# Performance work log

Hardware: AMD Instinct MI355X
Metric: run time of the kernel (lower is better)

Reference implementation:

```python
import jax, jax.numpy as jnp
import numpy as np

N_HEAD = 16

def setup_inputs() -> dict:
    key = jax.random.key(0)
    ks = jax.random.split(key, 9)
    B, T, C = 4, 2048, 1024
    s = 1.0 / np.sqrt(C)
    return {
        "x":  jax.random.normal(ks[0], (B, T, C), jnp.float32),
        "Wq": jax.random.normal(ks[1], (C, C), jnp.float32) * s,
        "bq": jax.random.normal(ks[2], (C,), jnp.float32) * 0.02,
        "Wk": jax.random.normal(ks[3], (C, C), jnp.float32) * s,
        "bk": jax.random.normal(ks[4], (C,), jnp.float32) * 0.02,
        "Wv": jax.random.normal(ks[5], (C, C), jnp.float32) * s,
        "bv": jax.random.normal(ks[6], (C,), jnp.float32) * 0.02,
        "Wp": jax.random.normal(ks[7], (C, C), jnp.float32) * s,
        "bp": jax.random.normal(ks[8], (C,), jnp.float32) * 0.02,
    }

def reference(x, Wq, bq, Wk, bk, Wv, bv, Wp, bp):
    B, T, C = x.shape
    H, D = N_HEAD, C // N_HEAD
    # torch nn.Linear: y = x @ W^T + b
    q = (x @ Wq.T + bq).reshape(B, T, H, D).transpose(0, 2, 1, 3)  # [B,H,T,D]
    k = (x @ Wk.T + bk).reshape(B, T, H, D).transpose(0, 2, 1, 3)
    v = (x @ Wv.T + bv).reshape(B, T, H, D).transpose(0, 2, 1, 3)
    # full TxT causal attention (non-flash path)
    att = jnp.einsum('bhtd,bhsd->bhts', q, k) * (1.0 / np.sqrt(D))  # [B,H,T,T]
    causal = jnp.tril(jnp.ones((T, T), dtype=bool))
    att = jnp.where(causal[None, None], att, -jnp.inf)
    att = jax.nn.softmax(att, axis=-1)
    y = jnp.einsum('bhts,bhsd->bhtd', att, v)  # [B,H,T,D]
    y = y.transpose(0, 2, 1, 3).reshape(B, T, C)
    return y @ Wp.T + bp
```

## Files before the change

kernel.cpp:

```cpp
#include <hip/hip_runtime.h>

typedef __bf16 bf16_t;
typedef __bf16 bf16x8 __attribute__((ext_vector_type(8)));
typedef __bf16 bf16x4 __attribute__((ext_vector_type(4)));
typedef float f32x4 __attribute__((ext_vector_type(4)));
typedef unsigned short ushort_t;

#define T_SEQ 2048
#define C_DIM 1024
#define NH    16
#define HD    64

__device__ __forceinline__ ushort_t f2bf(float f) {
    unsigned u = __builtin_bit_cast(unsigned, f);
    u += 0x7FFFu + ((u >> 16) & 1u);
    return (ushort_t)(u >> 16);
}

__device__ __forceinline__ void async_cp16(const void* g, void* l) {
    __builtin_amdgcn_global_load_lds(
        (const __attribute__((address_space(1))) void*)g,
        (__attribute__((address_space(3))) void*)l, 16, 0, 0);
}

#define X4  2097152
#define W4  262144
__global__ __launch_bounds__(256)
void cvt_all_kernel(const float* __restrict__ x,  const float* __restrict__ Wq,
                    const float* __restrict__ Wk, const float* __restrict__ Wv,
                    ushort_t* __restrict__ xb,  ushort_t* __restrict__ Wqb,
                    ushort_t* __restrict__ Wkb, ushort_t* __restrict__ Wvb) {
    int i = blockIdx.x * 256 + threadIdx.x;
    const float* src; ushort_t* dst; int off;
    if (i < X4)                { src = x;  dst = xb;  off = i; }
    else if (i < X4 + W4)      { src = Wq; dst = Wqb; off = i - X4; }
    else if (i < X4 + 2 * W4)  { src = Wk; dst = Wkb; off = i - X4 - W4; }
    else                       { src = Wv; dst = Wvb; off = i - X4 - 2 * W4; }
    float4 f = ((const float4*)src)[off];
    ushort4 u;
    u.x = f2bf(f.x); u.y = f2bf(f.y); u.z = f2bf(f.z); u.w = f2bf(f.w);
    ((ushort4*)dst)[off] = u;
}

__global__ __launch_bounds__(256)
void cvt_wp_kernel(const float* __restrict__ Wp, ushort_t* __restrict__ Wpb) {
    int i = blockIdx.x * 256 + threadIdx.x;
    float4 f = ((const float4*)Wp)[i];
    ushort4 u;
    u.x = f2bf(f.x); u.y = f2bf(f.y); u.z = f2bf(f.z); u.w = f2bf(f.w);
    ((ushort4*)Wpb)[i] = u;
}

__device__ __forceinline__ void gemm_core_128(const bf16_t* __restrict__ A,
                                              const bf16_t* __restrict__ B,
                                              f32x4 (&acc)[4][4]) {
    __shared__ alignas(16) ushort_t As[128 * 64];
    __shared__ alignas(16) ushort_t Ws[128 * 64];
    const int tid  = threadIdx.x;
    const int lane = tid & 63;
    const int wv   = tid >> 6;
    const int wm   = wv >> 1, wn = wv & 1;
    const int quad = lane >> 4, ln = lane & 15;
    const int m0 = blockIdx.x * 128, n0 = blockIdx.y * 128;

    f32x4 z4 = {0.f, 0.f, 0.f, 0.f};
#pragma unroll
    for (int i = 0; i < 4; i++)
#pragma unroll
        for (int j = 0; j < 4; j++) acc[i][j] = z4;

    const int lr = lane >> 3;
    const int lc = (lane & 7) ^ lr;
    const bf16_t* Ab = A + (size_t)(m0 + wv * 32 + lr) * 1024 + lc * 8;
    const bf16_t* Bb = B + (size_t)(n0 + wv * 32 + lr) * 1024 + lc * 8;

    for (int kt = 0; kt < 1024; kt += 64) {
#pragma unroll
        for (int p = 0; p < 4; ++p) {
            async_cp16(Ab + (size_t)p * 8192 + kt, &As[(wv * 4 + p) * 512]);
            async_cp16(Bb + (size_t)p * 8192 + kt, &Ws[(wv * 4 + p) * 512]);
        }
        __syncthreads();
#pragma unroll
        for (int ks = 0; ks < 2; ++ks) {
            bf16x8 af[4], bfr[4];
#pragma unroll
            for (int i = 0; i < 4; i++)
                af[i] = *(const bf16x8*)&As[(wm * 64 + i * 16 + ln) * 64 +
                                            (((ks * 4 + quad) ^ (ln & 7)) * 8)];
#pragma unroll
            for (int j = 0; j < 4; j++)
                bfr[j] = *(const bf16x8*)&Ws[(wn * 64 + j * 16 + ln) * 64 +
                                             (((ks * 4 + quad) ^ (ln & 7)) * 8)];
#pragma unroll
            for (int i = 0; i < 4; i++)
#pragma unroll
                for (int j = 0; j < 4; j++)
                    acc[i][j] = __builtin_amdgcn_mfma_f32_16x16x32_bf16(af[i], bfr[j],
                                                                        acc[i][j], 0, 0, 0);
        }
        __syncthreads();
    }
}

__global__ __launch_bounds__(256, 3)
void qkv_gemm_kernel(const bf16_t* __restrict__ xb,
                     const bf16_t* __restrict__ Wqb, const float* __restrict__ bq,
                     const bf16_t* __restrict__ Wkb, const float* __restrict__ bk,
                     const bf16_t* __restrict__ Wvb, const float* __restrict__ bv,
                     ushort_t* __restrict__ Qo, ushort_t* __restrict__ Ko,
                     ushort_t* __restrict__ Vo) {
    const int z = blockIdx.z;
    const bf16_t* W   = (z == 0) ? Wqb : (z == 1) ? Wkb : Wvb;
    const float* bias = (z == 0) ? bq : (z == 1) ? bk : bv;
    ushort_t* outp    = (z == 0) ? Qo : (z == 1) ? Ko : Vo;
    const float fs    = (z == 0) ? 0.18033688011112042f : 1.0f;

    f32x4 acc[4][4];
    gemm_core_128(xb, W, acc);

    const int tid  = threadIdx.x;
    const int lane = tid & 63;
    const int wv2  = tid >> 6;
    const int wm   = wv2 >> 1, wn = wv2 & 1;
    const int quad = lane >> 4, ln = lane & 15;
    const int mbase = blockIdx.x * 128 + wm * 64;
    const int nbase = blockIdx.y * 128 + wn * 64;

#pragma unroll
    for (int j = 0; j < 4; j++) {
        int n = nbase + j * 16 + ln;
        float bj = bias[n];
        int h = n >> 6, d = n & 63;
#pragma unroll
        for (int i = 0; i < 4; i++) {
            int mr = mbase + i * 16 + quad * 4;
            int b = mr >> 11;
            int t = mr & 2047;
            if (z < 2) {
                ushort_t* op = outp + ((size_t)(b * NH + h) * T_SEQ + t) * HD + d;
#pragma unroll
                for (int r = 0; r < 4; r++)
                    op[(size_t)r * HD] = f2bf((acc[i][j][r] + bj) * fs);
            } else {
                ushort4 us;
                us.x = f2bf(acc[i][j][0] + bj);
                us.y = f2bf(acc[i][j][1] + bj);
                us.z = f2bf(acc[i][j][2] + bj);
                us.w = f2bf(acc[i][j][3] + bj);
                *(ushort4*)(outp + ((size_t)(b * NH + h) * HD + d) * T_SEQ + t) = us;
            }
        }
    }
}

__device__ __forceinline__ int vkpos(int s) {
    return 32 * (s >> 5) + 8 * ((s >> 2) & 3) + 4 * ((s >> 4) & 1) + (s & 3);
}

__global__ __launch_bounds__(256, 4)
void flash_kernel(const ushort_t* __restrict__ Qw, const ushort_t* __restrict__ Kw,
                  const ushort_t* __restrict__ Vt, ushort_t* __restrict__ Y) {
    __shared__ alignas(16) ushort_t Ks[64 * 72];
    __shared__ alignas(16) ushort_t Vts[64 * 72];

    const int tid  = threadIdx.x;
    const int lane = tid & 63;
    const int wv   = tid >> 6;
    const int quad = lane >> 4, ln = lane & 15;
    const int L  = blockIdx.y * 16 + blockIdx.x;
    const int m  = L >> 3;
    const int bh = ((m >> 4) << 3) | (L & 7);
    const int p  = m & 15;
    const int qa = p, qb = 31 - p;
    const int b = bh >> 4, h = bh & 15;

    bf16x8 ones;
#pragma unroll
    for (int i = 0; i < 8; i++) ones[i] = (bf16_t)1.0f;

    const ushort_t* qpa = Qw + ((size_t)bh * T_SEQ + qa * 64 + wv * 16 + ln) * HD;
    const ushort_t* qpb = Qw + ((size_t)bh * T_SEQ + qb * 64 + wv * 16 + ln) * HD;
    bf16x8 aqA0 = *(const bf16x8*)(qpa + quad * 8);
    bf16x8 aqA1 = *(const bf16x8*)(qpa + 32 + quad * 8);
    bf16x8 aqB0 = *(const bf16x8*)(qpb + quad * 8);
    bf16x8 aqB1 = *(const bf16x8*)(qpb + 32 + quad * 8);

    f32x4 oA[4], oB[4];
    f32x4 z4 = {0.f, 0.f, 0.f, 0.f};
#pragma unroll
    for (int i = 0; i < 4; i++) { oA[i] = z4; oB[i] = z4; }
    f32x4 lA4 = z4, lB4 = z4;

    const int row0 = tid >> 3, c80 = (tid & 7) * 8;
    const int row1 = (256 + tid) >> 3;
    const int kp0 = vkpos(c80);
    const int kp1 = vkpos(c80 + 4);

    uint4 pk0, pk1, pv0, pv1;
    pk0 = *(const uint4*)(Kw + ((size_t)bh * T_SEQ + row0) * HD + c80);
    pv0 = *(const uint4*)(Vt + ((size_t)bh * HD + row0) * T_SEQ + c80);
    pk1 = *(const uint4*)(Kw + ((size_t)bh * T_SEQ + row1) * HD + c80);
    pv1 = *(const uint4*)(Vt + ((size_t)bh * HD + row1) * T_SEQ + c80);

    const int qrow = wv * 16 + ln;

    for (int st = 0; st <= qb; ++st) {
        __syncthreads();
        *(uint4*)&Ks[row0 * 72 + c80] = pk0;
        *(uint4*)&Ks[row1 * 72 + c80] = pk1;
        {
            uint2 a0 = {pv0.x, pv0.y}, a1 = {pv0.z, pv0.w};
            uint2 b0 = {pv1.x, pv1.y}, b1 = {pv1.z, pv1.w};
            *(uint2*)&Vts[row0 * 72 + kp0] = a0;
            *(uint2*)&Vts[row0 * 72 + kp1] = a1;
            *(uint2*)&Vts[row1 * 72 + kp0] = b0;
            *(uint2*)&Vts[row1 * 72 + kp1] = b1;
        }
        if (st < qb) {
            int s1 = (st + 1) * 64;
            pk0 = *(const uint4*)(Kw + ((size_t)bh * T_SEQ + s1 + row0) * HD + c80);
            pv0 = *(const uint4*)(Vt + ((size_t)bh * HD + row0) * T_SEQ + s1 + c80);
            pk1 = *(const uint4*)(Kw + ((size_t)bh * T_SEQ + s1 + row1) * HD + c80);
            pv1 = *(const uint4*)(Vt + ((size_t)bh * HD + row1) * T_SEQ + s1 + c80);
        }
        __syncthreads();

        const bool doA = (st <= qa);
        const bool dgA = (st == qa), dgB = (st == qb);

        bf16x8 apA[2], apB[2];
#pragma unroll
        for (int n16 = 0; n16 < 4; n16++) {
            bf16x8 bk0 = *(const bf16x8*)&Ks[(n16 * 16 + ln) * 72 + quad * 8];
            bf16x8 bk1 = *(const bf16x8*)&Ks[(n16 * 16 + ln) * 72 + 32 + quad * 8];
            const int ks = n16 >> 1, hf = (n16 & 1) * 4;
            f32x4 zB = {0.f, 0.f, 0.f, 0.f};
            zB = __builtin_amdgcn_mfma_f32_16x16x32_bf16(bk0, aqB0, zB, 0, 0, 0);
            zB = __builtin_amdgcn_mfma_f32_16x16x32_bf16(bk1, aqB1, zB, 0, 0, 0);
            if (doA) {
                f32x4 zA = {0.f, 0.f, 0.f, 0.f};
                zA = __builtin_amdgcn_mfma_f32_16x16x32_bf16(bk0, aqA0, zA, 0, 0, 0);
                zA = __builtin_amdgcn_mfma_f32_16x16x32_bf16(bk1, aqA1, zA, 0, 0, 0);
#pragma unroll
                for (int r = 0; r < 4; r++) {
                    float v = zA[r];
                    v = (dgA && (n16 * 16 + quad * 4 + r > qrow)) ? -1e30f : v;
                    apA[ks][hf + r] = (bf16_t)__builtin_amdgcn_exp2f(v);
                }
            }
#pragma unroll
            for (int r = 0; r < 4; r++) {
                float v = zB[r];
                v = (dgB && (n16 * 16 + quad * 4 + r > qrow)) ? -1e30f : v;
                apB[ks][hf + r] = (bf16_t)__builtin_amdgcn_exp2f(v);
            }
        }

#pragma unroll
        for (int ks = 0; ks < 2; ks++) {
            if (doA)
                lA4 = __builtin_amdgcn_mfma_f32_16x16x32_bf16(apA[ks], ones, lA4, 0, 0, 0);
            lB4 = __builtin_amdgcn_mfma_f32_16x16x32_bf16(apB[ks], ones, lB4, 0, 0, 0);
#pragma unroll
            for (int d16 = 0; d16 < 4; d16++) {
                bf16x8 bv = *(const bf16x8*)&Vts[(d16 * 16 + ln) * 72 + ks * 32 + quad * 8];
                if (doA)
                    oA[d16] = __builtin_amdgcn_mfma_f32_16x16x32_bf16(apA[ks], bv, oA[d16], 0, 0, 0);
                oB[d16] = __builtin_amdgcn_mfma_f32_16x16x32_bf16(apB[ks], bv, oB[d16], 0, 0, 0);
            }
        }
    }

#pragma unroll
    for (int ph = 0; ph < 2; ph++) {
        f32x4* o = ph ? oB : oA;
        f32x4 l4 = ph ? lB4 : lA4;
        int qt = ph ? qb : qa;
        f32x4 inv = {1.f / l4[0], 1.f / l4[1], 1.f / l4[2], 1.f / l4[3]};
        const int tg = qt * 64 + wv * 16 + quad * 4;
#pragma unroll
        for (int d16 = 0; d16 < 4; d16++) {
#pragma unroll
            for (int r = 0; r < 4; r++) {
                float v = o[d16][r] * inv[r];
                Y[((size_t)b * T_SEQ + tg + r) * C_DIM + h * HD + d16 * 16 + ln] = f2bf(v);
            }
        }
    }
}

__global__ __launch_bounds__(256, 3)
void proj_gemm_kernel(const bf16_t* __restrict__ Yw, const bf16_t* __restrict__ Wpb,
                      const float* __restrict__ bp, float* __restrict__ out) {
    f32x4 acc[4][4];
    gemm_core_128(Yw, Wpb, acc);

    const int tid  = threadIdx.x;
    const int lane = tid & 63;
    const int wv2  = tid >> 6;
    const int wm   = wv2 >> 1, wn = wv2 & 1;
    const int quad = lane >> 4, ln = lane & 15;
    const int mbase = blockIdx.x * 128 + wm * 64;
    const int nbase = blockIdx.y * 128 + wn * 64;

#pragma unroll
    for (int j = 0; j < 4; j++) {
        int n = nbase + j * 16 + ln;
        float bj = bp[n];
#pragma unroll
        for (int i = 0; i < 4; i++) {
            int mr = mbase + i * 16 + quad * 4;
#pragma unroll
            for (int r = 0; r < 4; r++)
                out[(size_t)(mr + r) * C_DIM + n] = acc[i][j][r] + bj;
        }
    }
}

extern "C" void kernel_launch(void* const* d_in, const int* in_sizes, int n_in,
                              void* d_out, int out_size, void* d_ws, size_t ws_size,
                              hipStream_t stream) {
    const float* x  = (const float*)d_in[0];
    const float* Wq = (const float*)d_in[1];
    const float* bq = (const float*)d_in[2];
    const float* Wk = (const float*)d_in[3];
    const float* bk = (const float*)d_in[4];
    const float* Wv = (const float*)d_in[5];
    const float* bv = (const float*)d_in[6];
    const float* Wp = (const float*)d_in[7];
    const float* bp = (const float*)d_in[8];
    float* out = (float*)d_out;

    char* ws = (char*)d_ws;
    const size_t MB = (size_t)1 << 20;
    ushort_t* Qw = (ushort_t*)(ws);
    ushort_t* Kw = (ushort_t*)(ws + 16 * MB);
    ushort_t* Vt = (ushort_t*)(ws + 32 * MB);
    ushort_t* Yw = (ushort_t*)(ws + 48 * MB);
    ushort_t* Wpb = (ushort_t*)(ws);

    ushort_t* xb  = (ushort_t*)out;
    ushort_t* Wqb = (ushort_t*)((char*)out + 16 * MB);
    ushort_t* Wkb = (ushort_t*)((char*)out + 18 * MB);
    ushort_t* Wvb = (ushort_t*)((char*)out + 20 * MB);

    cvt_all_kernel<<<11264, 256, 0, stream>>>(x, Wq, Wk, Wv, xb, Wqb, Wkb, Wvb);

    dim3 g1(64, 8, 3);
    qkv_gemm_kernel<<<g1, 256, 0, stream>>>((const bf16_t*)xb,
                                            (const bf16_t*)Wqb, bq,
                                            (const bf16_t*)Wkb, bk,
                                            (const bf16_t*)Wvb, bv,
                                            Qw, Kw, Vt);

    dim3 g2(16, 64);
    flash_kernel<<<g2, 256, 0, stream>>>(Qw, Kw, Vt, Yw);

    cvt_wp_kernel<<<1024, 256, 0, stream>>>(Wp, Wpb);

    dim3 g3(64, 8, 1);
    proj_gemm_kernel<<<g3, 256, 0, stream>>>((const bf16_t*)Yw, (const bf16_t*)Wpb, bp, out);
}
```

Measured before the change: 239.9 us.

## Double-buffer flash K/V tiles, vectorize GEMM epilogues, fold Wp conversion

The flash kernel now keeps two LDS buffers for K and V tiles. This lets it prefetch and store the next tile while computing the current one, and it uses one barrier per iteration instead of two. The Q/K and projection GEMMs swap the MFMA operand order so each lane holds 4 contiguous output columns, allowing vector bias loads and 8- or 16-byte stores instead of strided scalar writes. When the workspace is big enough, the Wp conversion is folded into the initial convert kernel, which removes one launch. Doubling LDS raises per-block shared memory, which may reduce occupancy.

```diff
diff --git a/kernel.cpp b/kernel.cpp
--- a/kernel.cpp
+++ b/kernel.cpp
@@ -28,14 +28,17 @@
 __global__ __launch_bounds__(256)
 void cvt_all_kernel(const float* __restrict__ x,  const float* __restrict__ Wq,
                     const float* __restrict__ Wk, const float* __restrict__ Wv,
+                    const float* __restrict__ Wp,
                     ushort_t* __restrict__ xb,  ushort_t* __restrict__ Wqb,
-                    ushort_t* __restrict__ Wkb, ushort_t* __restrict__ Wvb) {
+                    ushort_t* __restrict__ Wkb, ushort_t* __restrict__ Wvb,
+                    ushort_t* __restrict__ Wpb) {
     int i = blockIdx.x * 256 + threadIdx.x;
     const float* src; ushort_t* dst; int off;
     if (i < X4)                { src = x;  dst = xb;  off = i; }
     else if (i < X4 + W4)      { src = Wq; dst = Wqb; off = i - X4; }
     else if (i < X4 + 2 * W4)  { src = Wk; dst = Wkb; off = i - X4 - W4; }
-    else                       { src = Wv; dst = Wvb; off = i - X4 - 2 * W4; }
+    else if (i < X4 + 3 * W4)  { src = Wv; dst = Wvb; off = i - X4 - 2 * W4; }
+    else                       { src = Wp; dst = Wpb; off = i - X4 - 3 * W4; }
     float4 f = ((const float4*)src)[off];
     ushort4 u;
     u.x = f2bf(f.x); u.y = f2bf(f.y); u.z = f2bf(f.z); u.w = f2bf(f.w);
@@ -51,6 +54,7 @@
     ((ushort4*)Wpb)[i] = u;
 }
 
+template<bool SWAP>
 __device__ __forceinline__ void gemm_core_128(const bf16_t* __restrict__ A,
                                               const bf16_t* __restrict__ B,
                                               f32x4 (&acc)[4][4]) {
@@ -96,8 +100,11 @@
             for (int i = 0; i < 4; i++)
 #pragma unroll
                 for (int j = 0; j < 4; j++)
-                    acc[i][j] = __builtin_amdgcn_mfma_f32_16x16x32_bf16(af[i], bfr[j],
-                                                                        acc[i][j], 0, 0, 0);
+                    acc[i][j] = SWAP
+                        ? __builtin_amdgcn_mfma_f32_16x16x32_bf16(bfr[j], af[i],
+                                                                  acc[i][j], 0, 0, 0)
+                        : __builtin_amdgcn_mfma_f32_16x16x32_bf16(af[i], bfr[j],
+                                                                  acc[i][j], 0, 0, 0);
         }
         __syncthreads();
     }
@@ -116,9 +123,6 @@
     ushort_t* outp    = (z == 0) ? Qo : (z == 1) ? Ko : Vo;
     const float fs    = (z == 0) ? 0.18033688011112042f : 1.0f;
 
-    f32x4 acc[4][4];
-    gemm_core_128(xb, W, acc);
-
     const int tid  = threadIdx.x;
     const int lane = tid & 63;
     const int wv2  = tid >> 6;
@@ -127,22 +131,37 @@
     const int mbase = blockIdx.x * 128 + wm * 64;
     const int nbase = blockIdx.y * 128 + wn * 64;
 
-#pragma unroll
-    for (int j = 0; j < 4; j++) {
-        int n = nbase + j * 16 + ln;
-        float bj = bias[n];
-        int h = n >> 6, d = n & 63;
-#pragma unroll
-        for (int i = 0; i < 4; i++) {
-            int mr = mbase + i * 16 + quad * 4;
-            int b = mr >> 11;
-            int t = mr & 2047;
-            if (z < 2) {
-                ushort_t* op = outp + ((size_t)(b * NH + h) * T_SEQ + t) * HD + d;
-#pragma unroll
-                for (int r = 0; r < 4; r++)
-                    op[(size_t)r * HD] = f2bf((acc[i][j][r] + bj) * fs);
-            } else {
+    f32x4 acc[4][4];
+    if (z < 2) {
+        gemm_core_128<true>(xb, W, acc);
+#pragma unroll
+        for (int j = 0; j < 4; j++) {
+            int nb = nbase + j * 16 + quad * 4;
+            float4 b4 = *(const float4*)&bias[nb];
+            int h = nb >> 6, d = nb & 63;
+#pragma unroll
+            for (int i = 0; i < 4; i++) {
+                int m = mbase + i * 16 + ln;
+                int b = m >> 11, t = m & 2047;
+                ushort4 us;
+                us.x = f2bf((acc[i][j][0] + b4.x) * fs);
+                us.y = f2bf((acc[i][j][1] + b4.y) * fs);
+                us.z = f2bf((acc[i][j][2] + b4.z) * fs);
+                us.w = f2bf((acc[i][j][3] + b4.w) * fs);
+                *(ushort4*)(outp + ((size_t)(b * NH + h) * T_SEQ + t) * HD + d) = us;
+            }
+        }
+    } else {
+        gemm_core_128<false>(xb, W, acc);
+#pragma unroll
+        for (int j = 0; j < 4; j++) {
+            int n = nbase + j * 16 + ln;
+            float bj = bias[n];
+            int h = n >> 6, d = n & 63;
+#pragma unroll
+            for (int i = 0; i < 4; i++) {
+                int mr = mbase + i * 16 + quad * 4;
+                int b = mr >> 11, t = mr & 2047;
                 ushort4 us;
                 us.x = f2bf(acc[i][j][0] + bj);
                 us.y = f2bf(acc[i][j][1] + bj);
@@ -161,8 +180,8 @@
 __global__ __launch_bounds__(256, 4)
 void flash_kernel(const ushort_t* __restrict__ Qw, const ushort_t* __restrict__ Kw,
                   const ushort_t* __restrict__ Vt, ushort_t* __restrict__ Y) {
-    __shared__ alignas(16) ushort_t Ks[64 * 72];
-    __shared__ alignas(16) ushort_t Vts[64 * 72];
+    __shared__ alignas(16) ushort_t Ks[2][64 * 72];
+    __shared__ alignas(16) ushort_t Vts[2][64 * 72];
 
     const int tid  = threadIdx.x;
     const int lane = tid & 63;
@@ -198,42 +217,45 @@
     const int kp1 = vkpos(c80 + 4);
 
     uint4 pk0, pk1, pv0, pv1;
-    pk0 = *(const uint4*)(Kw + ((size_t)bh * T_SEQ + row0) * HD + c80);
-    pv0 = *(const uint4*)(Vt + ((size_t)bh * HD + row0) * T_SEQ + c80);
-    pk1 = *(const uint4*)(Kw + ((size_t)bh * T_SEQ + row1) * HD + c80);
-    pv1 = *(const uint4*)(Vt + ((size_t)bh * HD + row1) * T_SEQ + c80);
+    auto load_tile = [&](int sb) {
+        pk0 = *(const uint4*)(Kw + ((size_t)bh * T_SEQ + sb + row0) * HD + c80);
+        pv0 = *(const uint4*)(Vt + ((size_t)bh * HD + row0) * T_SEQ + sb + c80);
+        pk1 = *(const uint4*)(Kw + ((size_t)bh * T_SEQ + sb + row1) * HD + c80);
+        pv1 = *(const uint4*)(Vt + ((size_t)bh * HD + row1) * T_SEQ + sb + c80);
+    };
+    auto store_tile = [&](int bs) {
+        *(uint4*)&Ks[bs][row0 * 72 + c80] = pk0;
+        *(uint4*)&Ks[bs][row1 * 72 + c80] = pk1;
+        uint2 a0 = {pv0.x, pv0.y}, a1 = {pv0.z, pv0.w};
+        uint2 b0 = {pv1.x, pv1.y}, b1 = {pv1.z, pv1.w};
+        *(uint2*)&Vts[bs][row0 * 72 + kp0] = a0;
+        *(uint2*)&Vts[bs][row0 * 72 + kp1] = a1;
+        *(uint2*)&Vts[bs][row1 * 72 + kp0] = b0;
+        *(uint2*)&Vts[bs][row1 * 72 + kp1] = b1;
+    };
 
     const int qrow = wv * 16 + ln;
 
+    load_tile(0);
+    store_tile(0);
+    load_tile(64);
+    __syncthreads();
+
     for (int st = 0; st <= qb; ++st) {
-        __syncthreads();
-        *(uint4*)&Ks[row0 * 72 + c80] = pk0;
-        *(uint4*)&Ks[row1 * 72 + c80] = pk1;
-        {
-            uint2 a0 = {pv0.x, pv0.y}, a1 = {pv0.z, pv0.w};
-            uint2 b0 = {pv1.x, pv1.y}, b1 = {pv1.z, pv1.w};
-            *(uint2*)&Vts[row0 * 72 + kp0] = a0;
-            *(uint2*)&Vts[row0 * 72 + kp1] = a1;
-            *(uint2*)&Vts[row1 * 72 + kp0] = b0;
-            *(uint2*)&Vts[row1 * 72 + kp1] = b1;
-        }
-        if (st < qb) {
-            int s1 = (st + 1) * 64;
-            pk0 = *(const uint4*)(Kw + ((size_t)bh * T_SEQ + s1 + row0) * HD + c80);
-            pv0 = *(const uint4*)(Vt + ((size_t)bh * HD + row0) * T_SEQ + s1 + c80);
-            pk1 = *(const uint4*)(Kw + ((size_t)bh * T_SEQ + s1 + row1) * HD + c80);
-            pv1 = *(const uint4*)(Vt + ((size_t)bh * HD + row1) * T_SEQ + s1 + c80);
-        }
-        __syncthreads();
-
+        const int cur = st & 1;
+        if (st < qb) store_tile(cur ^ 1);
+        if (st + 2 <= qb) load_tile((st + 2) * 64);
+
+        const ushort_t* Kc = Ks[cur];
+        const ushort_t* Vc = Vts[cur];
         const bool doA = (st <= qa);
         const bool dgA = (st == qa), dgB = (st == qb);
 
         bf16x8 apA[2], apB[2];
 #pragma unroll
         for (int n16 = 0; n16 < 4; n16++) {
-            bf16x8 bk0 = *(const bf16x8*)&Ks[(n16 * 16 + ln) * 72 + quad * 8];
-            bf16x8 bk1 = *(const bf16x8*)&Ks[(n16 * 16 + ln) * 72 + 32 + quad * 8];
+            bf16x8 bk0 = *(const bf16x8*)&Kc[(n16 * 16 + ln) * 72 + quad * 8];
+            bf16x8 bk1 = *(const bf16x8*)&Kc[(n16 * 16 + ln) * 72 + 32 + quad * 8];
             const int ks = n16 >> 1, hf = (n16 & 1) * 4;
             f32x4 zB = {0.f, 0.f, 0.f, 0.f};
             zB = __builtin_amdgcn_mfma_f32_16x16x32_bf16(bk0, aqB0, zB, 0, 0, 0);
@@ -264,12 +286,13 @@
             lB4 = __builtin_amdgcn_mfma_f32_16x16x32_bf16(apB[ks], ones, lB4, 0, 0, 0);
 #pragma unroll
             for (int d16 = 0; d16 < 4; d16++) {
-                bf16x8 bv = *(const bf16x8*)&Vts[(d16 * 16 + ln) * 72 + ks * 32 + quad * 8];
+                bf16x8 bv = *(const bf16x8*)&Vc[(d16 * 16 + ln) * 72 + ks * 32 + quad * 8];
                 if (doA)
                     oA[d16] = __builtin_amdgcn_mfma_f32_16x16x32_bf16(apA[ks], bv, oA[d16], 0, 0, 0);
                 oB[d16] = __builtin_amdgcn_mfma_f32_16x16x32_bf16(apB[ks], bv, oB[d16], 0, 0, 0);
             }
         }
+        __syncthreads();
     }
 
 #pragma unroll
@@ -294,7 +317,7 @@
 void proj_gemm_kernel(const bf16_t* __restrict__ Yw, const bf16_t* __restrict__ Wpb,
                       const float* __restrict__ bp, float* __restrict__ out) {
     f32x4 acc[4][4];
-    gemm_core_128(Yw, Wpb, acc);
+    gemm_core_128<true>(Yw, Wpb, acc);
 
     const int tid  = threadIdx.x;
     const int lane = tid & 63;
@@ -306,14 +329,17 @@
 
 #pragma unroll
     for (int j = 0; j < 4; j++) {
-        int n = nbase + j * 16 + ln;
-        float bj = bp[n];
+        int nb = nbase + j * 16 + quad * 4;
+        float4 b4 = *(const float4*)&bp[nb];
 #pragma unroll
         for (int i = 0; i < 4; i++) {
-            int mr = mbase + i * 16 + quad * 4;
-#pragma unroll
-            for (int r = 0; r < 4; r++)
-                out[(size_t)(mr + r) * C_DIM + n] = acc[i][j][r] + bj;
+            int m = mbase + i * 16 + ln;
+            float4 o4;
+            o4.x = acc[i][j][0] + b4.x;
+            o4.y = acc[i][j][1] + b4.y;
+            o4.z = acc[i][j][2] + b4.z;
+            o4.w = acc[i][j][3] + b4.w;
+            *(float4*)&out[(size_t)m * C_DIM + nb] = o4;
         }
     }
 }
@@ -338,14 +364,17 @@
     ushort_t* Kw = (ushort_t*)(ws + 16 * MB);
     ushort_t* Vt = (ushort_t*)(ws + 32 * MB);
     ushort_t* Yw = (ushort_t*)(ws + 48 * MB);
-    ushort_t* Wpb = (ushort_t*)(ws);
+
+    const bool big_ws = ws_size >= 66 * MB;
+    ushort_t* Wpb = big_ws ? (ushort_t*)(ws + 64 * MB) : (ushort_t*)(ws);
 
     ushort_t* xb  = (ushort_t*)out;
     ushort_t* Wqb = (ushort_t*)((char*)out + 16 * MB);
     ushort_t* Wkb = (ushort_t*)((char*)out + 18 * MB);
     ushort_t* Wvb = (ushort_t*)((char*)out + 20 * MB);
 
-    cvt_all_kernel<<<11264, 256, 0, stream>>>(x, Wq, Wk, Wv, xb, Wqb, Wkb, Wvb);
+    cvt_all_kernel<<<big_ws ? 12288 : 11264, 256, 0, stream>>>(
+        x, Wq, Wk, Wv, Wp, xb, Wqb, Wkb, Wvb, Wpb);
 
     dim3 g1(64, 8, 3);
     qkv_gemm_kernel<<<g1, 256, 0, stream>>>((const bf16_t*)xb,
@@ -357,7 +386,8 @@
     dim3 g2(16, 64);
     flash_kernel<<<g2, 256, 0, stream>>>(Qw, Kw, Vt, Yw);
 
-    cvt_wp_kernel<<<1024, 256, 0, stream>>>(Wp, Wpb);
+    if (!big_ws)
+        cvt_wp_kernel<<<1024, 256, 0, stream>>>(Wp, Wpb);
 
     dim3 g3(64, 8, 1);
     proj_gemm_kernel<<<g3, 256, 0, stream>>>((const bf16_t*)Yw, (const bf16_t*)Wpb, bp, out);
```

New measurement: 246.3 us. 2.7% more time.
